# Performance work log

Measured on AMD Instinct MI355X. Metric: run time of the kernel, lower is better.

## Reference

```python
import jax, jax.numpy as jnp
import numpy as np

B = 4096      # batch
GH, GW = 13, 3
G = GH * GW   # 39 social grid cells
K = 20        # occupied cells per sample
T = 16        # history length
N = B * K     # total neighbors
FUT = 24      # decode horizon


def _lin_init(key, out_d, in_d):
    s = 1.0 / np.sqrt(in_d)
    kw, kb = jax.random.split(key)
    w = jax.random.uniform(kw, (out_d, in_d), jnp.float32, -s, s)
    b = jax.random.uniform(kb, (out_d,), jnp.float32, -s, s)
    return w, b


def setup_inputs() -> dict:
    key = jax.random.key(0)
    ks = jax.random.split(key, 12)
    x = jax.random.normal(ks[0], (B, 12, 24, 2), jnp.float32)
    beta = jax.random.uniform(ks[1], (B,), jnp.float32)
    context = jax.random.normal(ks[2], (T, B, 2), jnp.float32)
    nbrs = jax.random.normal(ks[3], (T, N, 2), jnp.float32)
    # first K of G grid cells occupied for every sample (deterministic pattern)
    cell = jnp.arange(G) < K                                  # (G,)
    mask = jnp.broadcast_to(cell[None, :, None], (B, G, 64)).reshape(B, GH, GW, 64)
    ip_w, ip_b = _lin_init(ks[4], 32, 2)
    enc_wih, enc_bih = _lin_init(ks[5], 4 * 64, 32)
    enc_whh, enc_bhh = _lin_init(ks[6], 4 * 64, 64)
    dyn_w, dyn_b = _lin_init(ks[7], 32, 64)
    lin1_w, lin1_b = _lin_init(ks[8], 1, 96)
    dec_wih, dec_bih = _lin_init(ks[9], 4 * 256, 96)
    dec_whh, dec_bhh = _lin_init(ks[10], 4 * 256, 256)
    op_w, op_b = _lin_init(ks[11], 5, 256)
    return dict(x=x, beta=beta, context=context, nbrs=nbrs, mask=mask,
                ip_w=ip_w, ip_b=ip_b, enc_wih=enc_wih, enc_whh=enc_whh,
                enc_bih=enc_bih, enc_bhh=enc_bhh, dyn_w=dyn_w, dyn_b=dyn_b,
                lin1_w=lin1_w, lin1_b=lin1_b, dec_wih=dec_wih, dec_whh=dec_whh,
                dec_bih=dec_bih, dec_bhh=dec_bhh, op_w=op_w, op_b=op_b)


def _lstm(seq, wih, whh, bih, bhh, hid):
    # seq: (T, n, in). torch gate order i, f, g, o. Returns (all_h, last_h).
    n = seq.shape[1]
    h0 = jnp.zeros((n, hid), seq.dtype)
    b = bih + bhh
    def step(carry, xt):
        h, c = carry
        g = xt @ wih.T + h @ whh.T + b
        i, f, gg, o = jnp.split(g, 4, axis=-1)
        c = jax.nn.sigmoid(f) * c + jax.nn.sigmoid(i) * jnp.tanh(gg)
        h = jax.nn.sigmoid(o) * jnp.tanh(c)
        return (h, c), h
    (h, c), hs = jax.lax.scan(step, (h0, h0), seq)
    return hs, h


def _lrelu(v):
    return jnp.where(v >= 0, v, 0.1 * v)


def _forward(x, beta, context, nbrs, mask,
             ip_w, ip_b, enc_wih, enc_whh, enc_bih, enc_bhh,
             dyn_w, dyn_b, lin1_w, lin1_b,
             dec_wih, dec_whh, dec_bih, dec_bhh, op_w, op_b):
    # --- encode ego history ---
    ctx_in = _lrelu(context @ ip_w.T + ip_b)            # (T, B, 32)
    _, hist_h = _lstm(ctx_in, enc_wih, enc_whh, enc_bih, enc_bhh, 64)  # (B, 64)
    hist_enc_one = _lrelu(hist_h @ dyn_w.T + dyn_b)     # (B, 32)
    # --- encode neighbors ---
    nbr_in = _lrelu(nbrs @ ip_w.T + ip_b)               # (T, N, 32)
    _, nbrs_h = _lstm(nbr_in, enc_wih, enc_whh, enc_bih, enc_bhh, 64)  # (N, 64)
    # --- masked_scatter_: place nbrs_h rows into True grid cells (row-major) ---
    b_, g_ = mask.shape[0], mask.shape[1] * mask.shape[2]
    cell_mask = mask.reshape(b_ * g_, mask.shape[3])[:, 0]            # (B*G,) bool
    idx = jnp.clip(jnp.cumsum(cell_mask.astype(jnp.int32)) - 1, 0, nbrs_h.shape[0] - 1)
    soc = jnp.where(cell_mask[:, None], nbrs_h[idx], 0.0).reshape(b_, g_, 64)
    mask_enc = cell_mask.reshape(b_, g_)                # (B, G)
    # --- tanh attention over grid cells ---
    hist_t = jnp.broadcast_to(hist_enc_one[:, None, :], (b_, g_, 32))
    new_hs = jnp.tanh(jnp.concatenate([hist_t, soc], axis=2))         # (B, G, 96)
    e = (new_hs @ lin1_w.T + lin1_b)[..., 0]            # (B, G)
    e = jnp.where(mask_enc, e, -1e9)
    attn = jax.nn.softmax(e, axis=1)
    enc = jnp.einsum('bg,bgc->bc', attn, soc)           # (B, 64)
    ctx = jnp.concatenate([hist_enc_one, enc], axis=1)  # (B, 96)
    # --- decode: repeat over 24 steps through dec_lstm ---
    dec_in = jnp.broadcast_to(ctx[None], (FUT, b_, 96))
    h_dec, _ = _lstm(dec_in, dec_wih, dec_whh, dec_bih, dec_bhh, 256)  # (24, B, 256)
    fut = h_dec @ op_w.T + op_b                         # (24, B, 5)
    mu = fut[..., :2]
    sig = jnp.exp(fut[..., 2:4])
    rho = jnp.tanh(fut[..., 4:5])
    out = jnp.concatenate([mu, sig, rho], axis=-1)      # (24, B, 5)
    return jnp.transpose(out, (1, 0, 2))                # (B, 24, 5)


def reference(x, beta, context, nbrs, mask,
              ip_w, ip_b, enc_wih, enc_whh, enc_bih, enc_bhh,
              dyn_w, dyn_b, lin1_w, lin1_b,
              dec_wih, dec_whh, dec_bih, dec_bhh, op_w, op_b):
    return _forward(x, beta, context, nbrs, mask,
                    ip_w, ip_b, enc_wih, enc_whh, enc_bih, enc_bhh,
                    dyn_w, dyn_b, lin1_w, lin1_b,
                    dec_wih, dec_whh, dec_bih, dec_bhh, op_w, op_b)
```

## Files before the change

### kernel.cpp

```cpp
#include <hip/hip_runtime.h>


#define S_TOT 86016
#define NB    4096
#define NNB   81920
#define TT    16
#define NFUT  24
#define HXS   104
#define L2E   1.44269504088896f

typedef __attribute__((ext_vector_type(8)))  short short8v;
typedef __attribute__((ext_vector_type(16))) float f32x16;

__device__ __forceinline__ float rcpf(float x) { return __builtin_amdgcn_rcpf(x); }
__device__ __forceinline__ float sigm2(float a)  { return rcpf(1.0f + exp2f(-a)); }
__device__ __forceinline__ float tanh2(float a)  { return 1.0f - 2.0f * rcpf(exp2f(a) + 1.0f); }
__device__ __forceinline__ float tanhx(float x)  { return tanh2(x * (2.0f * L2E)); }
__device__ __forceinline__ float lrelu(float v)  { return v >= 0.0f ? v : 0.1f * v; }
__device__ __forceinline__ short f2bf(float f) {
    unsigned u = __float_as_uint(f);
    unsigned r = (u + 0x7fffu + ((u >> 16) & 1u)) >> 16;
    return (short)r;
}

__device__ __forceinline__ void gl2lds(const short* g, short* l) {
    __builtin_amdgcn_global_load_lds(
        (const __attribute__((address_space(1))) void*)(g),
        (__attribute__((address_space(3))) void*)(l), 16, 0, 0);
}

__global__ __launch_bounds__(64) void k_pack_encB(
    const float* __restrict__ wih, const float* __restrict__ whh,
    const float* __restrict__ bih, const float* __restrict__ bhh,
    short* __restrict__ pB, float* __restrict__ pbias)
{
    const int fi = blockIdx.x;
    const int cc = fi % 6, gg = fi / 6;
    const int gate = gg & 3, H = gg >> 2;
    const int lane = threadIdx.x;
    const int row  = gate * 64 + H * 32 + (lane & 31);
    const float sc = (gate == 2) ? 2.0f * L2E : L2E;
    short8v v;
#pragma unroll
    for (int u = 0; u < 8; u++) {
        const int k = cc * 16 + (lane >> 5) * 8 + u;
        const float f = (k < 32) ? wih[row * 32 + k] : whh[row * 64 + (k - 32)];
        v[u] = f2bf(f * sc);
    }
    *(short8v*)&pB[((size_t)fi * 64 + lane) * 8] = v;
    if (cc == 0 && lane < 32)
        pbias[H * 128 + gate * 32 + lane] = (bih[row] + bhh[row]) * sc;
}

__global__ __launch_bounds__(256, 2) void k_encoder(
    const float* __restrict__ ctx_raw,
    const float* __restrict__ nbr_raw,
    const float* __restrict__ ipw, const float* __restrict__ ipb,
    const short* __restrict__ pB, const float* __restrict__ pbias,
    float* __restrict__ hfin)
{
    __shared__ short hx2[2 * 64 * HXS];
    const int tid  = threadIdx.x;
    const int lane = tid & 63;
    const int w    = __builtin_amdgcn_readfirstlane(tid >> 6);
    const int H    = w >> 1;
    const int M0   = (w & 1) * 32;
    const int seq_base = blockIdx.x * 64;
    const bool is_hist = (seq_base < NB);

    short8v Bf[4][6];
#pragma unroll
    for (int gate = 0; gate < 4; gate++)
#pragma unroll
        for (int cc = 0; cc < 6; cc++)
            Bf[gate][cc] = *(const short8v*)
                &pB[(((size_t)(H * 4 + gate) * 6 + cc) * 64 + lane) * 8];

    float b4[4];
#pragma unroll
    for (int gate = 0; gate < 4; gate++)
        b4[gate] = pbias[H * 128 + gate * 32 + (lane & 31)];

    {
        short8v z;
#pragma unroll
        for (int u = 0; u < 8; u++) z[u] = 0;
        for (int i = tid; i < 64 * 8; i += 256)
            *(short8v*)&hx2[(i >> 3) * HXS + 32 + (i & 7) * 8] = z;
    }

    const int sx = seq_base + (tid & 63);
    float2 f2;
    {
        const float* rp = is_hist ? &ctx_raw[(size_t)sx * 2]
                                  : &nbr_raw[(size_t)(sx - NB) * 2];
        f2 = *(const float2*)rp;
        const int k0 = (tid >> 6) * 8;
        short8v xv;
#pragma unroll
        for (int u = 0; u < 8; u++) {
            const int xj = k0 + u;
            xv[u] = f2bf(lrelu(ipb[xj] + ipw[xj * 2] * f2.x + ipw[xj * 2 + 1] * f2.y));
        }
        *(short8v*)&hx2[(tid & 63) * HXS + k0] = xv;
    }
    __syncthreads();

    float cst[16];
#pragma unroll
    for (int r = 0; r < 16; r++) cst[r] = 0.0f;

    const int aoff = (M0 + (lane & 31)) * HXS + (lane >> 5) * 8;
    const int hcol = 32 + H * 32 + (lane & 31);

#pragma unroll 1
    for (int t = 0; t < TT; t++) {
        short* cur = hx2 + (t & 1) * (64 * HXS);
        short* nxt = hx2 + ((t + 1) & 1) * (64 * HXS);

        float2 f2n = f2;
        if (t < TT - 1) {
            const float* rp = is_hist
                ? &ctx_raw[((size_t)(t + 1) * NB + sx) * 2]
                : &nbr_raw[((size_t)(t + 1) * NNB + (sx - NB)) * 2];
            f2n = *(const float2*)rp;
        }

        short8v Af[6];
#pragma unroll
        for (int cc = 0; cc < 6; cc++)
            Af[cc] = *(const short8v*)&cur[aoff + cc * 16];

        f32x16 C[4];
#pragma unroll
        for (int gate = 0; gate < 4; gate++)
#pragma unroll
            for (int r = 0; r < 16; r++) C[gate][r] = b4[gate];

#pragma unroll
        for (int cc = 0; cc < 6; cc++)
#pragma unroll
            for (int gate = 0; gate < 4; gate++)
                C[gate] = __builtin_amdgcn_mfma_f32_32x32x16_bf16(
                    Af[cc], Bf[gate][cc], C[gate], 0, 0, 0);

        float hn[16];
#pragma unroll
        for (int r = 0; r < 16; r++) {
            const float iv = sigm2(C[0][r]);
            const float fv = sigm2(C[1][r]);
            const float gv = tanh2(C[2][r]);
            const float ov = sigm2(C[3][r]);
            const float cn = fv * cst[r] + iv * gv;
            cst[r] = cn;
            hn[r] = ov * tanhx(cn);
        }

        if (t < TT - 1) {
#pragma unroll
            for (int r = 0; r < 16; r++) {
                const int row = (r & 3) + 8 * (r >> 2) + 4 * (lane >> 5);
                nxt[(M0 + row) * HXS + hcol] = f2bf(hn[r]);
            }
            const int k0 = (tid >> 6) * 8;
            short8v xv;
#pragma unroll
            for (int u = 0; u < 8; u++) {
                const int xj = k0 + u;
                xv[u] = f2bf(lrelu(ipb[xj] + ipw[xj * 2] * f2n.x + ipw[xj * 2 + 1] * f2n.y));
            }
            *(short8v*)&nxt[(tid & 63) * HXS + k0] = xv;
            __syncthreads();
            f2 = f2n;
        } else {
#pragma unroll
            for (int r = 0; r < 16; r++) {
                const int row = (r & 3) + 8 * (r >> 2) + 4 * (lane >> 5);
                hfin[(size_t)(seq_base + M0 + row) * 64 + H * 32 + (lane & 31)] = hn[r];
            }
        }
    }
}

__global__ __launch_bounds__(256) void k_attn(
    const float* __restrict__ h_enc,
    const float* __restrict__ dynw, const float* __restrict__ dynb,
    const float* __restrict__ l1w,  const float* __restrict__ l1b,
    float* __restrict__ ctx)
{
    const int b   = blockIdx.x;
    const int tid = threadIdx.x;
    __shared__ float sh_he[32];
    __shared__ float sh_soc[20][65];
    __shared__ float sh_e[20];

    if (tid < 32) {
        float a = dynb[tid];
        const float* w  = &dynw[tid * 64];
        const float* hb = &h_enc[(size_t)b * 64];
#pragma unroll 8
        for (int k = 0; k < 64; k++) a += w[k] * hb[k];
        a = lrelu(a);
        sh_he[tid] = a;
        ctx[b * 96 + tid] = a;
    }
    for (int idx = tid; idx < 20 * 64; idx += 256) {
        const int g = idx >> 6, k = idx & 63;
        sh_soc[g][k] = h_enc[(size_t)(NB + b * 20 + g) * 64 + k];
    }
    __syncthreads();

    if (tid < 20) {
        float e = l1b[0];
#pragma unroll
        for (int m = 0; m < 32; m++) e += l1w[m] * tanhx(sh_he[m]);
#pragma unroll 8
        for (int k = 0; k < 64; k++) e += l1w[32 + k] * tanhx(sh_soc[tid][k]);
        sh_e[tid] = e;
    }
    __syncthreads();

    if (tid < 64) {
        float mx = -1e30f;
#pragma unroll
        for (int g = 0; g < 20; g++) mx = fmaxf(mx, sh_e[g]);
        float wgt[20];
        float sm = 0.0f;
#pragma unroll
        for (int g = 0; g < 20; g++) { wgt[g] = exp2f((sh_e[g] - mx) * L2E); sm += wgt[g]; }
        const float inv = 1.0f / sm;
        float a = 0.0f;
#pragma unroll
        for (int g = 0; g < 20; g++) a += wgt[g] * sh_soc[g][tid];
        ctx[b * 96 + 32 + tid] = a * inv;
    }
}

__global__ __launch_bounds__(256) void k_pack_decB(
    const float* __restrict__ whh,
    const float* __restrict__ opw,
    short* __restrict__ pBd, short* __restrict__ opwB)
{
    const int bid  = blockIdx.x;
    const int tid  = threadIdx.x;
    const int lane = tid & 63;
    if (bid < 128) {
        const int gate = tid >> 6;
        const int hg = bid >> 4, cc = bid & 15;
        const int row  = gate * 256 + hg * 32 + (lane & 31);
        const int kb   = cc * 16 + (lane >> 5) * 8;
        const float sc = (gate == 2) ? 2.0f * L2E : L2E;
        short8v v;
#pragma unroll
        for (int u = 0; u < 8; u++) v[u] = f2bf(whh[row * 256 + kb + u] * sc);
        *(short8v*)&pBd[((size_t)(bid * 4 + gate) * 64 + lane) * 8] = v;
    } else if (tid < 64) {
        const int cc = bid - 128;
        const int n  = lane & 31, kb = cc * 16 + (lane >> 5) * 8;
        short8v v;
#pragma unroll
        for (int u = 0; u < 8; u++)
            v[u] = (n < 5) ? f2bf(opw[n * 256 + kb + u]) : (short)0;
        *(short8v*)&opwB[(cc * 64 + lane) * 8] = v;
    }
}

__global__ __launch_bounds__(256) void k_gx(
    const float* __restrict__ ctx,
    const float* __restrict__ wih,
    const float* __restrict__ bih, const float* __restrict__ bhh,
    float* __restrict__ pgx)
{
    const int lane = threadIdx.x & 63;
    const int s    = blockIdx.x * 64 + lane;
    const int jq   = __builtin_amdgcn_readfirstlane(blockIdx.y * 4 + (threadIdx.x >> 6));
    const int j0   = jq * 4;
    float acc[4];
#pragma unroll
    for (int d = 0; d < 4; d++) acc[d] = bih[j0 + d] + bhh[j0 + d];
    const float* c = &ctx[(size_t)s * 96];
    for (int k0 = 0; k0 < 96; k0 += 8) {
        float cb[8];
#pragma unroll
        for (int u = 0; u < 8; u++) cb[u] = c[k0 + u];
#pragma unroll
        for (int d = 0; d < 4; d++) {
            const float* w = &wih[(j0 + d) * 96 + k0];
#pragma unroll
            for (int u = 0; u < 8; u++) acc[d] += w[u] * cb[u];
        }
    }
#pragma unroll
    for (int d = 0; d < 4; d++) {
        const int row = j0 + d;
        const int g = row >> 8, j = row & 255;
        const float sc = (g == 2) ? 2.0f * L2E : L2E;
        pgx[(((size_t)s << 8) + j) * 4 + g] = acc[d] * sc;
    }
}

#define STAGE(ccv, bufv) do {                                              \
    const short* gs = wb + (size_t)(ccv) * 2048 + lane * 8;                \
    short* ls = &wstg[w][bufv][0];                                         \
    gl2lds(gs + 0,    ls + 0);                                             \
    gl2lds(gs + 512,  ls + 512);                                           \
    gl2lds(gs + 1024, ls + 1024);                                          \
    gl2lds(gs + 1536, ls + 1536);                                          \
} while (0)

#define DOCC(ccv, bufv, VMC, DOSTAGE) do {                                 \
    asm volatile("s_waitcnt vmcnt(" VMC ")" ::: "memory");                 \
    __builtin_amdgcn_sched_barrier(0);                                     \
    const short8v W0 = *(const short8v*)&wstg[w][bufv][0 * 512 + lane * 8];\
    const short8v W1 = *(const short8v*)&wstg[w][bufv][1 * 512 + lane * 8];\
    const short8v W2 = *(const short8v*)&wstg[w][bufv][2 * 512 + lane * 8];\
    const short8v W3 = *(const short8v*)&wstg[w][bufv][3 * 512 + lane * 8];\
    const short8v Af = *(const short8v*)                                   \
        (cur + n * 512 + (((ccv) * 32 + hl * 16) ^ ((n & 7) << 4)));       \
    short8v Of;                                                            \
    if (headw) Of = *(const short8v*)&ldsO[(ccv) * 512 + lane * 8];        \
    asm volatile("s_waitcnt lgkmcnt(0)" ::: "memory");                     \
    __builtin_amdgcn_sched_barrier(0);                                     \
    if (DOSTAGE) STAGE((ccv) + 2, bufv);                                   \
    C[0] = __builtin_amdgcn_mfma_f32_32x32x16_bf16(Af, W0, C[0], 0, 0, 0); \
    C[1] = __builtin_amdgcn_mfma_f32_32x32x16_bf16(Af, W1, C[1], 0, 0, 0); \
    C[2] = __builtin_amdgcn_mfma_f32_32x32x16_bf16(Af, W2, C[2], 0, 0, 0); \
    C[3] = __builtin_amdgcn_mfma_f32_32x32x16_bf16(Af, W3, C[3], 0, 0, 0); \
    if (headw)                                                             \
        Ch = __builtin_amdgcn_mfma_f32_32x32x16_bf16(Af, Of, Ch, 0, 0, 0); \
} while (0)

__global__ __launch_bounds__(512, 1) void k_dec_persist(
    const float* __restrict__ pgx,
    const short* __restrict__ pBd,
    const short* __restrict__ opwB,
    const float* __restrict__ opb,
    float* __restrict__ out)
{
    __shared__ short hbuf[2][32 * 256];
    __shared__ short wstg[8][2][2048];
    __shared__ short ldsO[16 * 512];
    const int tid  = threadIdx.x;
    const int lane = tid & 63;
    const int w    = __builtin_amdgcn_readfirstlane(tid >> 6);
    const int Ab   = blockIdx.x * 32;
    const int n    = lane & 31;
    const int hl   = lane >> 5;
    const bool headw = (w == 0);

    const short* wb = pBd + (size_t)w * 32768;

    if (headw) {
#pragma unroll
        for (int i = 0; i < 16; i++)
            gl2lds(opwB + i * 512 + lane * 8, &ldsO[i * 512]);
    }

    float cst[16];
#pragma unroll
    for (int r = 0; r < 16; r++) cst[r] = 0.0f;

#pragma unroll 1
    for (int t = 0; t < NFUT; t++) {
        const char* cur = (const char*)hbuf[t & 1];
        char* nxt       = (char*)hbuf[(t + 1) & 1];

        f32x16 C[4], Ch;
#pragma unroll
        for (int g = 0; g < 4; g++)
#pragma unroll
            for (int r = 0; r < 16; r++) C[g][r] = 0.0f;
#pragma unroll
        for (int r = 0; r < 16; r++) Ch[r] = 0.0f;

        if (t > 0) {
            STAGE(0, 0);
            STAGE(1, 1);
#pragma unroll 1
            for (int c2 = 0; c2 < 14; c2 += 2) {
                DOCC(c2,     0, "4", 1);
                DOCC(c2 + 1, 1, "4", 1);
            }
            DOCC(14, 0, "4", 0);
            DOCC(15, 1, "0", 0);
        }

#pragma unroll
        for (int r = 0; r < 16; r++) {
            const int al = (r & 3) + 8 * (r >> 2) + 4 * hl;
            const float4 g4 = *(const float4*)
                &pgx[(((size_t)(Ab + al) << 8) + w * 32 + n) * 4];
            const float iv = sigm2(C[0][r] + g4.x);
            const float fv = sigm2(C[1][r] + g4.y);
            const float gv = tanh2(C[2][r] + g4.z);
            const float ov = sigm2(C[3][r] + g4.w);
            const float cn = fv * cst[r] + iv * gv;
            cst[r] = cn;
            const int hbyte = al * 512 + (((w * 32 + n) * 2) ^ ((al & 7) << 4));
            *(short*)(nxt + hbyte) = f2bf(ov * tanhx(cn));
        }

        if (t > 0 && headw && n < 5) {
            const float obias = opb[n];
#pragma unroll
            for (int r = 0; r < 16; r++) {
                const int agent = Ab + (r & 3) + 8 * (r >> 2) + 4 * hl;
                float v = Ch[r] + obias;
                if (n == 2 || n == 3) v = exp2f(v * L2E);
                else if (n == 4) v = tanhx(v);
                out[(size_t)agent * (NFUT * 5) + (t - 1) * 5 + n] = v;
            }
        }

        __syncthreads();
    }

    if (headw) {
        const char* cur = (const char*)hbuf[NFUT & 1];
        f32x16 Ch;
#pragma unroll
        for (int r = 0; r < 16; r++) Ch[r] = 0.0f;
#pragma unroll 4
        for (int cc = 0; cc < 16; cc++) {
            const int abyte = n * 512 + ((cc * 32 + hl * 16) ^ ((n & 7) << 4));
            const short8v Af = *(const short8v*)(cur + abyte);
            const short8v Of = *(const short8v*)&ldsO[cc * 512 + lane * 8];
            Ch = __builtin_amdgcn_mfma_f32_32x32x16_bf16(Af, Of, Ch, 0, 0, 0);
        }
        if (n < 5) {
            const float obias = opb[n];
#pragma unroll
            for (int r = 0; r < 16; r++) {
                const int agent = Ab + (r & 3) + 8 * (r >> 2) + 4 * hl;
                float v = Ch[r] + obias;
                if (n == 2 || n == 3) v = exp2f(v * L2E);
                else if (n == 4) v = tanhx(v);
                out[(size_t)agent * (NFUT * 5) + (NFUT - 1) * 5 + n] = v;
            }
        }
    }
}

extern "C" void kernel_launch(void* const* d_in, const int* in_sizes, int n_in,
                              void* d_out, int out_size, void* d_ws, size_t ws_size,
                              hipStream_t stream)
{
    const float* ctx_raw = (const float*)d_in[2];
    const float* nbr_raw = (const float*)d_in[3];
    const float* ipw     = (const float*)d_in[5];
    const float* ipb     = (const float*)d_in[6];
    const float* enc_wih = (const float*)d_in[7];
    const float* enc_whh = (const float*)d_in[8];
    const float* enc_bih = (const float*)d_in[9];
    const float* enc_bhh = (const float*)d_in[10];
    const float* dynw    = (const float*)d_in[11];
    const float* dynb    = (const float*)d_in[12];
    const float* l1w     = (const float*)d_in[13];
    const float* l1b     = (const float*)d_in[14];
    const float* dec_wih = (const float*)d_in[15];
    const float* dec_whh = (const float*)d_in[16];
    const float* dec_bih = (const float*)d_in[17];
    const float* dec_bhh = (const float*)d_in[18];
    const float* opw     = (const float*)d_in[19];
    const float* opb     = (const float*)d_in[20];
    float* out = (float*)d_out;

    char* pc = (char*)d_ws;
    float* hfin  = (float*)pc; pc += (size_t)S_TOT * 64 * 4;
    float* ctxb  = (float*)pc; pc += (size_t)NB * 96 * 4;
    float* pgx   = (float*)pc; pc += (size_t)NB * 1024 * 4;
    float* pbias = (float*)pc; pc += 256 * 4;
    short* pB    = (short*)pc; pc += (size_t)48 * 64 * 8 * 2;
    short* pBd   = (short*)pc; pc += (size_t)8 * 16 * 4 * 64 * 8 * 2;
    short* opwB  = (short*)pc; pc += (size_t)16 * 64 * 8 * 2;

    k_pack_encB<<<dim3(48), 64, 0, stream>>>(enc_wih, enc_whh, enc_bih, enc_bhh,
                                             pB, pbias);
    k_pack_decB<<<dim3(144), 256, 0, stream>>>(dec_whh, opw, pBd, opwB);

    k_encoder<<<dim3(S_TOT / 64), 256, 0, stream>>>(
        ctx_raw, nbr_raw, ipw, ipb, pB, pbias, hfin);

    k_attn<<<dim3(NB), 256, 0, stream>>>(hfin, dynw, dynb, l1w, l1b, ctxb);

    k_gx<<<dim3(NB / 64, 64), 256, 0, stream>>>(ctxb, dec_wih, dec_bih, dec_bhh, pgx);

    k_dec_persist<<<dim3(NB / 32), 512, 0, stream>>>(pgx, pBd, opwB, opb, out);
}
```

Before: 577.7 us.

## Halve decoder agents per block and switch to 16x16x32 MFMA tiles

```diff
diff --git a/kernel.cpp b/kernel.cpp
--- a/kernel.cpp
+++ b/kernel.cpp
@@ -11,6 +11,7 @@
 
 typedef __attribute__((ext_vector_type(8)))  short short8v;
 typedef __attribute__((ext_vector_type(16))) float f32x16;
+typedef __attribute__((ext_vector_type(4)))  float f32x4v;
 
 __device__ __forceinline__ float rcpf(float x) { return __builtin_amdgcn_rcpf(x); }
 __device__ __forceinline__ float sigm2(float a)  { return rcpf(1.0f + exp2f(-a)); }
@@ -236,32 +237,33 @@
     }
 }
 
-__global__ __launch_bounds__(256) void k_pack_decB(
+__global__ __launch_bounds__(512) void k_pack_decB2(
     const float* __restrict__ whh,
     const float* __restrict__ opw,
-    short* __restrict__ pBd, short* __restrict__ opwB)
+    short* __restrict__ pBd2, short* __restrict__ opwB2)
 {
     const int bid  = blockIdx.x;
     const int tid  = threadIdx.x;
     const int lane = tid & 63;
-    if (bid < 128) {
-        const int gate = tid >> 6;
-        const int hg = bid >> 4, cc = bid & 15;
-        const int row  = gate * 256 + hg * 32 + (lane & 31);
-        const int kb   = cc * 16 + (lane >> 5) * 8;
+    if (bid < 64) {
+        const int hg = bid >> 3, kc = bid & 7;
+        const int frag = tid >> 6;
+        const int nt = frag >> 2, gate = frag & 3;
+        const int row = gate * 256 + hg * 32 + nt * 16 + (lane & 15);
+        const int kb  = kc * 32 + ((lane >> 4) & 3) * 8;
         const float sc = (gate == 2) ? 2.0f * L2E : L2E;
         short8v v;
 #pragma unroll
         for (int u = 0; u < 8; u++) v[u] = f2bf(whh[row * 256 + kb + u] * sc);
-        *(short8v*)&pBd[((size_t)(bid * 4 + gate) * 64 + lane) * 8] = v;
+        *(short8v*)&pBd2[((size_t)(bid * 8 + frag) * 64 + lane) * 8] = v;
     } else if (tid < 64) {
-        const int cc = bid - 128;
-        const int n  = lane & 31, kb = cc * 16 + (lane >> 5) * 8;
+        const int kc = bid - 64;
+        const int n  = lane & 15, kb = kc * 32 + ((lane >> 4) & 3) * 8;
         short8v v;
 #pragma unroll
         for (int u = 0; u < 8; u++)
             v[u] = (n < 5) ? f2bf(opw[n * 256 + kb + u]) : (short)0;
-        *(short8v*)&opwB[(cc * 64 + lane) * 8] = v;
+        *(short8v*)&opwB2[(kc * 64 + lane) * 8] = v;
     }
 }
 
@@ -299,116 +301,142 @@
     }
 }
 
-#define STAGE(ccv, bufv) do {                                              \
-    const short* gs = wb + (size_t)(ccv) * 2048 + lane * 8;                \
+#define STAGE8(kcv, bufv) do {                                             \
+    const short* gs = wb + (size_t)(kcv) * 4096 + lane * 8;                \
     short* ls = &wstg[w][bufv][0];                                         \
     gl2lds(gs + 0,    ls + 0);                                             \
     gl2lds(gs + 512,  ls + 512);                                           \
     gl2lds(gs + 1024, ls + 1024);                                          \
     gl2lds(gs + 1536, ls + 1536);                                          \
+    gl2lds(gs + 2048, ls + 2048);                                          \
+    gl2lds(gs + 2560, ls + 2560);                                          \
+    gl2lds(gs + 3072, ls + 3072);                                          \
+    gl2lds(gs + 3584, ls + 3584);                                          \
 } while (0)
 
-#define DOCC(ccv, bufv, VMC, DOSTAGE) do {                                 \
-    asm volatile("s_waitcnt vmcnt(" VMC ")" ::: "memory");                 \
-    __builtin_amdgcn_sched_barrier(0);                                     \
-    const short8v W0 = *(const short8v*)&wstg[w][bufv][0 * 512 + lane * 8];\
-    const short8v W1 = *(const short8v*)&wstg[w][bufv][1 * 512 + lane * 8];\
-    const short8v W2 = *(const short8v*)&wstg[w][bufv][2 * 512 + lane * 8];\
-    const short8v W3 = *(const short8v*)&wstg[w][bufv][3 * 512 + lane * 8];\
-    const short8v Af = *(const short8v*)                                   \
-        (cur + n * 512 + (((ccv) * 32 + hl * 16) ^ ((n & 7) << 4)));       \
-    short8v Of;                                                            \
-    if (headw) Of = *(const short8v*)&ldsO[(ccv) * 512 + lane * 8];        \
-    asm volatile("s_waitcnt lgkmcnt(0)" ::: "memory");                     \
-    __builtin_amdgcn_sched_barrier(0);                                     \
-    if (DOSTAGE) STAGE((ccv) + 2, bufv);                                   \
-    C[0] = __builtin_amdgcn_mfma_f32_32x32x16_bf16(Af, W0, C[0], 0, 0, 0); \
-    C[1] = __builtin_amdgcn_mfma_f32_32x32x16_bf16(Af, W1, C[1], 0, 0, 0); \
-    C[2] = __builtin_amdgcn_mfma_f32_32x32x16_bf16(Af, W2, C[2], 0, 0, 0); \
-    C[3] = __builtin_amdgcn_mfma_f32_32x32x16_bf16(Af, W3, C[3], 0, 0, 0); \
-    if (headw)                                                             \
-        Ch = __builtin_amdgcn_mfma_f32_32x32x16_bf16(Af, Of, Ch, 0, 0, 0); \
+#define DOCC8(kcv, bufv, VMC, DOSTAGE) do {                                 \
+    asm volatile("s_waitcnt vmcnt(" VMC ")" ::: "memory");                  \
+    __builtin_amdgcn_sched_barrier(0);                                      \
+    const short8v W0 = *(const short8v*)&wstg[w][bufv][0 * 512 + lane * 8]; \
+    const short8v W1 = *(const short8v*)&wstg[w][bufv][1 * 512 + lane * 8]; \
+    const short8v W2 = *(const short8v*)&wstg[w][bufv][2 * 512 + lane * 8]; \
+    const short8v W3 = *(const short8v*)&wstg[w][bufv][3 * 512 + lane * 8]; \
+    const short8v W4 = *(const short8v*)&wstg[w][bufv][4 * 512 + lane * 8]; \
+    const short8v W5 = *(const short8v*)&wstg[w][bufv][5 * 512 + lane * 8]; \
+    const short8v W6 = *(const short8v*)&wstg[w][bufv][6 * 512 + lane * 8]; \
+    const short8v W7 = *(const short8v*)&wstg[w][bufv][7 * 512 + lane * 8]; \
+    const short8v Af = *(const short8v*)                                    \
+        (cur + rowA * 512 + (((kcv) * 64 + kg * 16) ^ ((rowA & 7) << 4)));  \
+    short8v Of;                                                             \
+    if (headw) Of = *(const short8v*)&ldsO[(kcv) * 512 + lane * 8];         \
+    asm volatile("s_waitcnt lgkmcnt(0)" ::: "memory");                      \
+    __builtin_amdgcn_sched_barrier(0);                                      \
+    if (DOSTAGE) STAGE8((kcv) + 2, bufv);                                   \
+    C00 = __builtin_amdgcn_mfma_f32_16x16x32_bf16(Af, W0, C00, 0, 0, 0);    \
+    C01 = __builtin_amdgcn_mfma_f32_16x16x32_bf16(Af, W1, C01, 0, 0, 0);    \
+    C02 = __builtin_amdgcn_mfma_f32_16x16x32_bf16(Af, W2, C02, 0, 0, 0);    \
+    C03 = __builtin_amdgcn_mfma_f32_16x16x32_bf16(Af, W3, C03, 0, 0, 0);    \
+    C10 = __builtin_amdgcn_mfma_f32_16x16x32_bf16(Af, W4, C10, 0, 0, 0);    \
+    C11 = __builtin_amdgcn_mfma_f32_16x16x32_bf16(Af, W5, C11, 0, 0, 0);    \
+    C12 = __builtin_amdgcn_mfma_f32_16x16x32_bf16(Af, W6, C12, 0, 0, 0);    \
+    C13 = __builtin_amdgcn_mfma_f32_16x16x32_bf16(Af, W7, C13, 0, 0, 0);    \
+    if (headw)                                                              \
+        Ch4 = __builtin_amdgcn_mfma_f32_16x16x32_bf16(Af, Of, Ch4, 0, 0, 0);\
 } while (0)
 
 __global__ __launch_bounds__(512, 1) void k_dec_persist(
     const float* __restrict__ pgx,
-    const short* __restrict__ pBd,
-    const short* __restrict__ opwB,
+    const short* __restrict__ pBd2,
+    const short* __restrict__ opwB2,
     const float* __restrict__ opb,
     float* __restrict__ out)
 {
-    __shared__ short hbuf[2][32 * 256];
-    __shared__ short wstg[8][2][2048];
-    __shared__ short ldsO[16 * 512];
+    __shared__ short hbuf[2][16 * 256];
+    __shared__ short wstg[8][2][4096];
+    __shared__ short ldsO[8 * 512];
     const int tid  = threadIdx.x;
     const int lane = tid & 63;
     const int w    = __builtin_amdgcn_readfirstlane(tid >> 6);
-    const int Ab   = blockIdx.x * 32;
-    const int n    = lane & 31;
-    const int hl   = lane >> 5;
+    const int Ab   = blockIdx.x * 16;
+    const int rowA = lane & 15;
+    const int kg   = (lane >> 4) & 3;
     const bool headw = (w == 0);
 
-    const short* wb = pBd + (size_t)w * 32768;
+    const short* wb = pBd2 + (size_t)w * 32768;
 
     if (headw) {
 #pragma unroll
-        for (int i = 0; i < 16; i++)
-            gl2lds(opwB + i * 512 + lane * 8, &ldsO[i * 512]);
-    }
-
-    float cst[16];
-#pragma unroll
-    for (int r = 0; r < 16; r++) cst[r] = 0.0f;
+        for (int i = 0; i < 8; i++)
+            gl2lds(opwB2 + i * 512 + lane * 8, &ldsO[i * 512]);
+    }
+
+    float cst[8];
+#pragma unroll
+    for (int r = 0; r < 8; r++) cst[r] = 0.0f;
 
 #pragma unroll 1
     for (int t = 0; t < NFUT; t++) {
         const char* cur = (const char*)hbuf[t & 1];
         char* nxt       = (char*)hbuf[(t + 1) & 1];
 
-        f32x16 C[4], Ch;
-#pragma unroll
-        for (int g = 0; g < 4; g++)
-#pragma unroll
-            for (int r = 0; r < 16; r++) C[g][r] = 0.0f;
-#pragma unroll
-        for (int r = 0; r < 16; r++) Ch[r] = 0.0f;
+        f32x4v C00 = {0,0,0,0}, C01 = {0,0,0,0}, C02 = {0,0,0,0}, C03 = {0,0,0,0};
+        f32x4v C10 = {0,0,0,0}, C11 = {0,0,0,0}, C12 = {0,0,0,0}, C13 = {0,0,0,0};
+        f32x4v Ch4 = {0,0,0,0};
 
         if (t > 0) {
-            STAGE(0, 0);
-            STAGE(1, 1);
-#pragma unroll 1
-            for (int c2 = 0; c2 < 14; c2 += 2) {
-                DOCC(c2,     0, "4", 1);
-                DOCC(c2 + 1, 1, "4", 1);
-            }
-            DOCC(14, 0, "4", 0);
-            DOCC(15, 1, "0", 0);
-        }
-
-#pragma unroll
-        for (int r = 0; r < 16; r++) {
-            const int al = (r & 3) + 8 * (r >> 2) + 4 * hl;
-            const float4 g4 = *(const float4*)
-                &pgx[(((size_t)(Ab + al) << 8) + w * 32 + n) * 4];
-            const float iv = sigm2(C[0][r] + g4.x);
-            const float fv = sigm2(C[1][r] + g4.y);
-            const float gv = tanh2(C[2][r] + g4.z);
-            const float ov = sigm2(C[3][r] + g4.w);
-            const float cn = fv * cst[r] + iv * gv;
-            cst[r] = cn;
-            const int hbyte = al * 512 + (((w * 32 + n) * 2) ^ ((al & 7) << 4));
-            *(short*)(nxt + hbyte) = f2bf(ov * tanhx(cn));
-        }
-
-        if (t > 0 && headw && n < 5) {
-            const float obias = opb[n];
-#pragma unroll
-            for (int r = 0; r < 16; r++) {
-                const int agent = Ab + (r & 3) + 8 * (r >> 2) + 4 * hl;
-                float v = Ch[r] + obias;
-                if (n == 2 || n == 3) v = exp2f(v * L2E);
-                else if (n == 4) v = tanhx(v);
-                out[(size_t)agent * (NFUT * 5) + (t - 1) * 5 + n] = v;
+            STAGE8(0, 0);
+            STAGE8(1, 1);
+            DOCC8(0, 0, "8", 1);
+            DOCC8(1, 1, "8", 1);
+            DOCC8(2, 0, "8", 1);
+            DOCC8(3, 1, "8", 1);
+            DOCC8(4, 0, "8", 1);
+            DOCC8(5, 1, "8", 1);
+            DOCC8(6, 0, "8", 0);
+            DOCC8(7, 1, "0", 0);
+        }
+
+#pragma unroll
+        for (int r = 0; r < 4; r++) {
+            const int al = kg * 4 + r;
+            {
+                const int j = w * 32 + (lane & 15);
+                const float4 g4 = *(const float4*)
+                    &pgx[(((size_t)(Ab + al) << 8) + j) * 4];
+                const float iv = sigm2(C00[r] + g4.x);
+                const float fv = sigm2(C01[r] + g4.y);
+                const float gv = tanh2(C02[r] + g4.z);
+                const float ov = sigm2(C03[r] + g4.w);
+                const float cn = fv * cst[r] + iv * gv;
+                cst[r] = cn;
+                const int hbyte = al * 512 + ((j * 2) ^ ((al & 7) << 4));
+                *(short*)(nxt + hbyte) = f2bf(ov * tanhx(cn));
+            }
+            {
+                const int j = w * 32 + 16 + (lane & 15);
+                const float4 g4 = *(const float4*)
+                    &pgx[(((size_t)(Ab + al) << 8) + j) * 4];
+                const float iv = sigm2(C10[r] + g4.x);
+                const float fv = sigm2(C11[r] + g4.y);
+                const float gv = tanh2(C12[r] + g4.z);
+                const float ov = sigm2(C13[r] + g4.w);
+                const float cn = fv * cst[4 + r] + iv * gv;
+                cst[4 + r] = cn;
+                const int hbyte = al * 512 + ((j * 2) ^ ((al & 7) << 4));
+                *(short*)(nxt + hbyte) = f2bf(ov * tanhx(cn));
+            }
+        }
+
+        if (t > 0 && headw && (lane & 15) < 5) {
+            const int o = lane & 15;
+            const float obias = opb[o];
+#pragma unroll
+            for (int r = 0; r < 4; r++) {
+                const int agent = Ab + kg * 4 + r;
+                float v = Ch4[r] + obias;
+                if (o == 2 || o == 3) v = exp2f(v * L2E);
+                else if (o == 4) v = tanhx(v);
+                out[(size_t)agent * (NFUT * 5) + (t - 1) * 5 + o] = v;
             }
         }
 
@@ -417,25 +445,24 @@
 
     if (headw) {
         const char* cur = (const char*)hbuf[NFUT & 1];
-        f32x16 Ch;
-#pragma unroll
-        for (int r = 0; r < 16; r++) Ch[r] = 0.0f;
-#pragma unroll 4
-        for (int cc = 0; cc < 16; cc++) {
-            const int abyte = n * 512 + ((cc * 32 + hl * 16) ^ ((n & 7) << 4));
+        f32x4v Ch = {0, 0, 0, 0};
+#pragma unroll
+        for (int kc = 0; kc < 8; kc++) {
+            const int abyte = rowA * 512 + ((kc * 64 + kg * 16) ^ ((rowA & 7) << 4));
             const short8v Af = *(const short8v*)(cur + abyte);
-            const short8v Of = *(const short8v*)&ldsO[cc * 512 + lane * 8];
-            Ch = __builtin_amdgcn_mfma_f32_32x32x16_bf16(Af, Of, Ch, 0, 0, 0);
-        }
-        if (n < 5) {
-            const float obias = opb[n];
-#pragma unroll
-            for (int r = 0; r < 16; r++) {
-                const int agent = Ab + (r & 3) + 8 * (r >> 2) + 4 * hl;
+            const short8v Of = *(const short8v*)&ldsO[kc * 512 + lane * 8];
+            Ch = __builtin_amdgcn_mfma_f32_16x16x32_bf16(Af, Of, Ch, 0, 0, 0);
+        }
+        if ((lane & 15) < 5) {
+            const int o = lane & 15;
+            const float obias = opb[o];
+#pragma unroll
+            for (int r = 0; r < 4; r++) {
+                const int agent = Ab + kg * 4 + r;
                 float v = Ch[r] + obias;
-                if (n == 2 || n == 3) v = exp2f(v * L2E);
-                else if (n == 4) v = tanhx(v);
-                out[(size_t)agent * (NFUT * 5) + (NFUT - 1) * 5 + n] = v;
+                if (o == 2 || o == 3) v = exp2f(v * L2E);
+                else if (o == 4) v = tanhx(v);
+                out[(size_t)agent * (NFUT * 5) + (NFUT - 1) * 5 + o] = v;
             }
         }
     }
@@ -471,12 +498,12 @@
     float* pgx   = (float*)pc; pc += (size_t)NB * 1024 * 4;
     float* pbias = (float*)pc; pc += 256 * 4;
     short* pB    = (short*)pc; pc += (size_t)48 * 64 * 8 * 2;
-    short* pBd   = (short*)pc; pc += (size_t)8 * 16 * 4 * 64 * 8 * 2;
-    short* opwB  = (short*)pc; pc += (size_t)16 * 64 * 8 * 2;
+    short* pBd2  = (short*)pc; pc += (size_t)64 * 8 * 64 * 8 * 2;
+    short* opwB2 = (short*)pc; pc += (size_t)8 * 64 * 8 * 2;
 
     k_pack_encB<<<dim3(48), 64, 0, stream>>>(enc_wih, enc_whh, enc_bih, enc_bhh,
                                              pB, pbias);
-    k_pack_decB<<<dim3(144), 256, 0, stream>>>(dec_whh, opw, pBd, opwB);
+    k_pack_decB2<<<dim3(72), 512, 0, stream>>>(dec_whh, opw, pBd2, opwB2);
 
     k_encoder<<<dim3(S_TOT / 64), 256, 0, stream>>>(
         ctx_raw, nbr_raw, ipw, ipb, pB, pbias, hfin);
@@ -485,5 +512,5 @@
 
     k_gx<<<dim3(NB / 64, 64), 256, 0, stream>>>(ctxb, dec_wih, dec_bih, dec_bhh, pgx);
 
-    k_dec_persist<<<dim3(NB / 32), 512, 0, stream>>>(pgx, pBd, opwB, opb, out);
-}
+    k_dec_persist<<<dim3(NB / 16), 512, 0, stream>>>(pgx, pBd2, opwB2, opb, out);
+}
```

Measured after the change: 629.2 us. 8.9% more time.
